# Kernel optimization log

Measured on AMD Instinct MI355X. Metric: run time of the kernel, lower is better.

Reference implementation:

```python
import jax, jax.numpy as jnp
import numpy as np

N = 60000      # total nodes (disjoint batch)
E = 240000     # total edges
F_IN = 10      # node feature dim
S = 3          # edge feature dim
C = 16         # nNodes (channel width)
G = 512        # number of graphs in batch


def setup_inputs() -> dict:
    key = jax.random.key(0)
    ks = jax.random.split(key, 24)
    sc = 0.05
    inp = {
        "x": jax.random.normal(ks[0], (N, F_IN), jnp.float32),
        "a_vals": jax.random.uniform(ks[1], (E,), jnp.float32),
        "e": jax.random.normal(ks[2], (E, S), jnp.float32),
        "edge_index": jax.random.randint(ks[3], (2, E), 0, N, jnp.int32),
        "seg": jnp.sort(jax.random.randint(ks[4], (N,), 0, G, jnp.int32)),
        # GCNConv 1/2
        "W_gcn1": jax.random.normal(ks[5], (F_IN, C), jnp.float32) * sc,
        "b_gcn1": jnp.zeros((C,), jnp.float32),
        "W_gcn2": jax.random.normal(ks[6], (C, 2 * C), jnp.float32) * sc,
        "b_gcn2": jnp.zeros((2 * C,), jnp.float32),
        # ECCConv 1 (edge kernel net: Dense(S -> F_IN*C), root kernel, bias)
        "We1": jax.random.normal(ks[7], (S, F_IN * C), jnp.float32) * sc,
        "be1": jnp.zeros((F_IN * C,), jnp.float32),
        "root1": jax.random.normal(ks[8], (F_IN, C), jnp.float32) * sc,
        "bias1": jnp.zeros((C,), jnp.float32),
        # ECCConv 2 (Dense(S -> C*2C))
        "We2": jax.random.normal(ks[9], (S, C * 2 * C), jnp.float32) * sc,
        "be2": jnp.zeros((C * 2 * C,), jnp.float32),
        "root2": jax.random.normal(ks[10], (C, 2 * C), jnp.float32) * sc,
        "bias2": jnp.zeros((2 * C,), jnp.float32),
        # MLP head: concat(2C + 2C) -> C -> C//2 -> 1
        "Wd1": jax.random.normal(ks[11], (4 * C, C), jnp.float32) * sc,
        "bd1": jnp.zeros((C,), jnp.float32),
        "Wd2": jax.random.normal(ks[12], (C, C // 2), jnp.float32) * sc,
        "bd2": jnp.zeros((C // 2,), jnp.float32),
        "Wo": jax.random.normal(ks[13], (C // 2, 1), jnp.float32) * sc,
        "bo": jnp.zeros((1,), jnp.float32),
    }
    return inp


def _spmm(rows, cols, vals, y):
    # sparse A @ y : out[i] += vals * y[j]
    return jax.ops.segment_sum(vals[:, None] * y[cols], rows, num_segments=N)


def _gcn(x, rows, cols, vals, W, b):
    return jax.nn.relu(_spmm(rows, cols, vals, x @ W) + b)


def _ecc(x, rows, cols, e, We, be, root, bias, f_in, f_out):
    # per-edge kernel matrix from edge features
    kern = (e @ We + be).reshape(-1, f_in, f_out)        # [E, Fin, Fout]
    msgs = jnp.einsum('ef,efo->eo', x[cols], kern)       # [E, Fout]
    agg = jax.ops.segment_sum(msgs, rows, num_segments=N)
    return jax.nn.relu(agg + x @ root + bias)


def reference(x, a_vals, e, edge_index, seg,
              W_gcn1, b_gcn1, W_gcn2, b_gcn2,
              We1, be1, root1, bias1,
              We2, be2, root2, bias2,
              Wd1, bd1, Wd2, bd2, Wo, bo):
    rows, cols = edge_index[0], edge_index[1]
    # GCN branch
    g1 = _gcn(x, rows, cols, a_vals, W_gcn1, b_gcn1)      # [N, C]
    g2 = _gcn(g1, rows, cols, a_vals, W_gcn2, b_gcn2)     # [N, 2C]
    # ECC branch
    c1 = _ecc(x, rows, cols, e, We1, be1, root1, bias1, F_IN, C)       # [N, C]
    c2 = _ecc(c1, rows, cols, e, We2, be2, root2, bias2, C, 2 * C)     # [N, 2C]
    # global sum pool per graph
    p1 = jax.ops.segment_sum(g2, seg, num_segments=G)     # [G, 2C]
    p2 = jax.ops.segment_sum(c2, seg, num_segments=G)     # [G, 2C]
    h = jnp.concatenate([p1, p2], axis=-1)                # [G, 4C]
    h = jax.nn.relu(h @ Wd1 + bd1)
    h = jax.nn.relu(h @ Wd2 + bd2)
    # dropout rate 0.0 -> identity (inference)
    return jax.nn.sigmoid(h @ Wo + bo)                    # [G, 1]
```

## Files before the change

### kernel.cpp

```cpp
#include <hip/hip_runtime.h>
#include <math.h>

#define N_NODES 60000
#define N_EDGES 240000
#define F_INQ 10
#define G_DIM 512
#define CAP 32
#define NB_EDGE ((N_EDGES + 255) / 256)
#define NB_TILE ((N_NODES + 63) / 64)
#define NB_E1  ((N_NODES * F_INQ + 255) / 256)
#define PQ1_STRIDE 56

__global__ __launch_bounds__(256) void k_build(
    const int* __restrict__ ei, const float* __restrict__ a_vals,
    const float* __restrict__ efeat,
    int* __restrict__ rs, int* __restrict__ ecol, float4* __restrict__ edata,
    const float* __restrict__ Wg1, const float* __restrict__ bg1,
    const float* __restrict__ We1, const float* __restrict__ be1,
    const float* __restrict__ root1, const float* __restrict__ bias1,
    const float* __restrict__ Wg2, const float* __restrict__ bg2,
    const float* __restrict__ We2, const float* __restrict__ be2,
    const float* __restrict__ root2, const float* __restrict__ bias2,
    float* __restrict__ Wt1, float* __restrict__ Wt2)
{
    if (blockIdx.x == NB_EDGE) {
        for (int i = threadIdx.x; i < 16 * 11; i += 256) {
            int o = i / 11, f = i - o * 11;
            Wt1[o * 64 + f] = (f < 10) ? Wg1[f * 16 + o] : bg1[o];
        }
        for (int i = threadIdx.x; i < 16 * 51; i += 256) {
            int o = i / 51, f = i - o * 51;
            float w;
            if      (f < 10) w = be1[f * 16 + o];
            else if (f < 20) w = We1[(f - 10) * 16 + o];
            else if (f < 30) w = We1[160 + (f - 20) * 16 + o];
            else if (f < 40) w = We1[320 + (f - 30) * 16 + o];
            else if (f < 50) w = root1[(f - 40) * 16 + o];
            else             w = bias1[o];
            Wt1[(16 + o) * 64 + f] = w;
        }
        return;
    }
    if (blockIdx.x == NB_EDGE + 1) {
        for (int i = threadIdx.x; i < 32 * 17; i += 256) {
            int o = i / 17, f = i - o * 17;
            Wt2[o * 96 + f] = (f < 16) ? Wg2[f * 32 + o] : bg2[o];
        }
        for (int i = threadIdx.x; i < 32 * 81; i += 256) {
            int o = i / 81, f = i - o * 81;
            float w;
            if      (f < 16) w = be2[f * 32 + o];
            else if (f < 32) w = We2[(f - 16) * 32 + o];
            else if (f < 48) w = We2[512 + (f - 32) * 32 + o];
            else if (f < 64) w = We2[1024 + (f - 48) * 32 + o];
            else if (f < 80) w = root2[(f - 64) * 32 + o];
            else             w = bias2[o];
            Wt2[(32 + o) * 96 + f] = w;
        }
        return;
    }

    int e = blockIdx.x * 256 + threadIdx.x;
    if (e >= N_EDGES) return;
    int row = ei[e];
    int slot = atomicAdd(&rs[row], 1);
    int idx = row * CAP + slot;
    ecol[idx] = ei[N_EDGES + e];
    edata[idx] = make_float4(a_vals[e], efeat[e * 3], efeat[e * 3 + 1], efeat[e * 3 + 2]);
}

__global__ __launch_bounds__(256) void k_edge1(
    const float* __restrict__ x,
    const int* __restrict__ rs,
    const int* __restrict__ ecol, const float4* __restrict__ edata,
    float* __restrict__ PQ1)
{
    int idx = blockIdx.x * 256 + threadIdx.x;
    if (idx >= N_NODES * F_INQ) return;
    int node = idx / F_INQ;
    int f = idx - node * F_INQ;
    int start = node * CAP;
    int end = start + rs[node];
    float p0 = 0.f, p1 = 0.f, p2 = 0.f, p3 = 0.f, q = 0.f;
    int k = start;
    for (; k + 2 <= end; k += 2) {
        int c0 = ecol[k], c1 = ecol[k + 1];
        float4 e0 = edata[k], e1 = edata[k + 1];
        float x0 = x[c0 * F_INQ + f];
        float x1 = x[c1 * F_INQ + f];
        p0 += x0;        p0 += x1;
        p1 += e0.y * x0; p1 += e1.y * x1;
        p2 += e0.z * x0; p2 += e1.z * x1;
        p3 += e0.w * x0; p3 += e1.w * x1;
        q  += e0.x * x0; q  += e1.x * x1;
    }
    if (k < end) {
        int c0 = ecol[k];
        float4 e0 = edata[k];
        float x0 = x[c0 * F_INQ + f];
        p0 += x0;
        p1 += e0.y * x0;
        p2 += e0.z * x0;
        p3 += e0.w * x0;
        q  += e0.x * x0;
    }
    float* P = PQ1 + (size_t)node * PQ1_STRIDE;
    P[f]      = p0;
    P[10 + f] = p1;
    P[20 + f] = p2;
    P[30 + f] = p3;
    P[40 + f] = q;
}

__global__ __launch_bounds__(256) void k_tf1(
    const float* __restrict__ PQ1,
    const float* __restrict__ x,
    const float* __restrict__ Wt1,
    float* __restrict__ gc)
{
    __shared__ float val[64][33];
    int tile = blockIdx.x;
    int lane = threadIdx.x & 63;
    int wv = __builtin_amdgcn_readfirstlane(threadIdx.x >> 6);
    int node = tile * 64 + lane;
    int nclamp = node < N_NODES ? node : N_NODES - 1;

    float pr[52];
    const float4* P4 = (const float4*)(PQ1 + (size_t)nclamp * PQ1_STRIDE);
#pragma unroll
    for (int i = 0; i < 13; ++i) {
        float4 t = P4[i];
        pr[i * 4] = t.x; pr[i * 4 + 1] = t.y; pr[i * 4 + 2] = t.z; pr[i * 4 + 3] = t.w;
    }
    float xs[10];
    const float2* X2 = (const float2*)(x + (size_t)nclamp * F_INQ);
#pragma unroll
    for (int i = 0; i < 5; ++i) {
        float2 t = X2[i];
        xs[i * 2] = t.x; xs[i * 2 + 1] = t.y;
    }

#pragma unroll
    for (int j = 0; j < 4; ++j) {
        const float* wr = Wt1 + (wv * 4 + j) * 64;
        float a = wr[10];
#pragma unroll
        for (int f = 0; f < 10; ++f) a = fmaf(wr[f], pr[40 + f], a);
        val[lane][(wv * 4 + j) * 2] = a > 0.f ? a : 0.f;
    }
#pragma unroll
    for (int j = 0; j < 4; ++j) {
        const float* wr = Wt1 + (16 + wv * 4 + j) * 64;
        float a = wr[50];
#pragma unroll
        for (int f = 0; f < 40; ++f) a = fmaf(wr[f], pr[f], a);
#pragma unroll
        for (int f = 0; f < 10; ++f) a = fmaf(wr[40 + f], xs[f], a);
        val[lane][(wv * 4 + j) * 2 + 1] = a > 0.f ? a : 0.f;
    }
    __syncthreads();

    float4* G4 = (float4*)(gc + (size_t)tile * 64 * 32);
#pragma unroll
    for (int k = 0; k < 2; ++k) {
        int fi4 = k * 256 + threadIdx.x;
        int n = fi4 >> 3, o4 = (fi4 & 7) * 4;
        if (tile * 64 + n < N_NODES)
            G4[fi4] = make_float4(val[n][o4], val[n][o4 + 1], val[n][o4 + 2], val[n][o4 + 3]);
    }
}

__global__ __launch_bounds__(256) void k_edge2(
    const float* __restrict__ gc,
    const int* __restrict__ rs,
    const int* __restrict__ ecol, const float4* __restrict__ edata,
    float* __restrict__ PQ2)
{
    int idx = blockIdx.x * 256 + threadIdx.x;
    int node = idx >> 4, f = idx & 15;
    int start = node * CAP;
    int end = start + rs[node];
    const float2* GC2 = (const float2*)gc;
    float p0 = 0.f, p1 = 0.f, p2 = 0.f, p3 = 0.f, q = 0.f;
    int k = start;
    for (; k + 2 <= end; k += 2) {
        int c0 = ecol[k], c1 = ecol[k + 1];
        float4 e0 = edata[k], e1 = edata[k + 1];
        float2 t0 = GC2[c0 * 16 + f];
        float2 t1 = GC2[c1 * 16 + f];
        p0 += t0.y;        p0 += t1.y;
        p1 += e0.y * t0.y; p1 += e1.y * t1.y;
        p2 += e0.z * t0.y; p2 += e1.z * t1.y;
        p3 += e0.w * t0.y; p3 += e1.w * t1.y;
        q  += e0.x * t0.x; q  += e1.x * t1.x;
    }
    if (k < end) {
        int c0 = ecol[k];
        float4 e0 = edata[k];
        float2 t0 = GC2[c0 * 16 + f];
        p0 += t0.y;
        p1 += e0.y * t0.y;
        p2 += e0.z * t0.y;
        p3 += e0.w * t0.y;
        q  += e0.x * t0.x;
    }
    float* P = PQ2 + (size_t)node * 80;
    P[f]      = p0;
    P[16 + f] = p1;
    P[32 + f] = p2;
    P[48 + f] = p3;
    P[64 + f] = q;
}

__global__ __launch_bounds__(256) void k_tf2pool(
    const float* __restrict__ PQ2,
    const float* __restrict__ gc,
    const int* __restrict__ seg,
    const float* __restrict__ Wt2,
    float* __restrict__ pool)
{
    __shared__ float val[64][65];
    __shared__ int sseg[64];
    int tile = blockIdx.x;
    int lane = threadIdx.x & 63;
    int wv = __builtin_amdgcn_readfirstlane(threadIdx.x >> 6);
    int node = tile * 64 + lane;
    int nclamp = node < N_NODES ? node : N_NODES - 1;

    if (threadIdx.x < 64) {
        int nd = tile * 64 + threadIdx.x;
        sseg[threadIdx.x] = (nd < N_NODES) ? seg[nd] : -1;
    }

    float pr[80];
    const float4* P4 = (const float4*)(PQ2 + (size_t)nclamp * 80);
#pragma unroll
    for (int i = 0; i < 20; ++i) {
        float4 t = P4[i];
        pr[i * 4] = t.x; pr[i * 4 + 1] = t.y; pr[i * 4 + 2] = t.z; pr[i * 4 + 3] = t.w;
    }
    float cs[16];
    const float4* C4 = (const float4*)(gc + (size_t)nclamp * 32);
#pragma unroll
    for (int i = 0; i < 8; ++i) {
        float4 t = C4[i];
        cs[i * 2] = t.y; cs[i * 2 + 1] = t.w;
    }

#pragma unroll
    for (int j = 0; j < 8; ++j) {
        const float* wr = Wt2 + (wv * 8 + j) * 96;
        float a = wr[16];
#pragma unroll
        for (int f = 0; f < 16; ++f) a = fmaf(wr[f], pr[64 + f], a);
        val[lane][wv * 8 + j] = a > 0.f ? a : 0.f;
    }
#pragma unroll
    for (int j = 0; j < 8; ++j) {
        const float* wr = Wt2 + (32 + wv * 8 + j) * 96;
        float a = wr[80];
#pragma unroll
        for (int f = 0; f < 64; ++f) a = fmaf(wr[f], pr[f], a);
#pragma unroll
        for (int f = 0; f < 16; ++f) a = fmaf(wr[64 + f], cs[f], a);
        val[lane][32 + wv * 8 + j] = a > 0.f ? a : 0.f;
    }
    __syncthreads();

    int c = threadIdx.x & 63, q = threadIdx.x >> 6;
    int base = q * 16;
    float acc = 0.f;
    int curg = -1;
    for (int n = 0; n < 16; ++n) {
        int nd = tile * 64 + base + n;
        if (nd >= N_NODES) break;
        int gsg = sseg[base + n];
        if (gsg != curg) {
            if (curg >= 0) atomicAdd(&pool[curg * 64 + c], acc);
            acc = 0.f;
            curg = gsg;
        }
        acc += val[base + n][c];
    }
    if (curg >= 0) atomicAdd(&pool[curg * 64 + c], acc);
}

__global__ __launch_bounds__(256) void k_head(
    const float* __restrict__ pool,
    const float* __restrict__ Wd1, const float* __restrict__ bd1,
    const float* __restrict__ Wd2, const float* __restrict__ bd2,
    const float* __restrict__ Wo,  const float* __restrict__ bo,
    float* __restrict__ out)
{
    __shared__ float pl[4][64];
    __shared__ float h1s[4][16];
    __shared__ float h2s[4][8];
    int q = threadIdx.x >> 6, t = threadIdx.x & 63;
    int g = blockIdx.x * 4 + q;
    pl[q][t] = pool[g * 64 + t];
    __syncthreads();
    if (t < 16) {
        float a = bd1[t];
        for (int k = 0; k < 64; ++k) a += pl[q][k] * Wd1[k * 16 + t];
        h1s[q][t] = a > 0.f ? a : 0.f;
    }
    __syncthreads();
    if (t < 8) {
        float a = bd2[t];
        for (int k = 0; k < 16; ++k) a += h1s[q][k] * Wd2[k * 8 + t];
        h2s[q][t] = a > 0.f ? a : 0.f;
    }
    __syncthreads();
    if (t == 0) {
        float a = bo[0];
        for (int k = 0; k < 8; ++k) a += h2s[q][k] * Wo[k];
        out[g] = 1.f / (1.f + expf(-a));
    }
}

extern "C" void kernel_launch(void* const* d_in, const int* in_sizes, int n_in,
                              void* d_out, int out_size, void* d_ws, size_t ws_size,
                              hipStream_t stream)
{
    const float* x      = (const float*)d_in[0];
    const float* a_vals = (const float*)d_in[1];
    const float* efeat  = (const float*)d_in[2];
    const int*   ei     = (const int*)d_in[3];
    const int*   seg    = (const int*)d_in[4];
    const float* Wg1    = (const float*)d_in[5];
    const float* bg1    = (const float*)d_in[6];
    const float* Wg2    = (const float*)d_in[7];
    const float* bg2    = (const float*)d_in[8];
    const float* We1    = (const float*)d_in[9];
    const float* be1    = (const float*)d_in[10];
    const float* root1  = (const float*)d_in[11];
    const float* bias1  = (const float*)d_in[12];
    const float* We2    = (const float*)d_in[13];
    const float* be2    = (const float*)d_in[14];
    const float* root2  = (const float*)d_in[15];
    const float* bias2  = (const float*)d_in[16];
    const float* Wd1    = (const float*)d_in[17];
    const float* bd1    = (const float*)d_in[18];
    const float* Wd2    = (const float*)d_in[19];
    const float* bd2    = (const float*)d_in[20];
    const float* Wo     = (const float*)d_in[21];
    const float* bo     = (const float*)d_in[22];

    float4* edata = (float4*)d_ws;
    float*  PQ1  = (float*)(edata + (size_t)N_NODES * CAP);
    float*  gc   = PQ1 + (size_t)N_NODES * PQ1_STRIDE;
    float*  PQ2  = gc + (size_t)N_NODES * 32;
    float*  Wt1  = PQ2 + (size_t)N_NODES * 80;
    float*  Wt2  = Wt1 + 32 * 64;
    int*    rs   = (int*)(Wt2 + 64 * 96);
    float*  pool = (float*)(rs + N_NODES);
    int*    ecol = (int*)(pool + (size_t)G_DIM * 64);
    float*  out  = (float*)d_out;

    hipMemsetAsync(rs, 0, sizeof(int) * (N_NODES + G_DIM * 64), stream);

    k_build<<<NB_EDGE + 2, 256, 0, stream>>>(ei, a_vals, efeat, rs, ecol, edata,
                                             Wg1, bg1, We1, be1, root1, bias1,
                                             Wg2, bg2, We2, be2, root2, bias2,
                                             Wt1, Wt2);

    k_edge1<<<NB_E1, 256, 0, stream>>>(x, rs, ecol, edata, PQ1);
    k_tf1  <<<NB_TILE, 256, 0, stream>>>(PQ1, x, Wt1, gc);

    k_edge2<<<N_NODES * 16 / 256, 256, 0, stream>>>(gc, rs, ecol, edata, PQ2);
    k_tf2pool<<<NB_TILE, 256, 0, stream>>>(PQ2, gc, seg, Wt2, pool);

    k_head<<<G_DIM / 4, 256, 0, stream>>>(pool, Wd1, bd1, Wd2, bd2, Wo, bo, out);
}
```

Baseline: 178.5 us.

## Fuse layer-1 edge aggregation and node transform into one kernel

Merges k_edge1 and k_tf1 into a single k_l1 kernel. Each node is handled by a 16-lane group: lanes gather the per-feature aggregates, then exchange them through shuffles to compute the 16 GCN and 16 ECC outputs directly. Layer-1 weights are staged in shared memory per block, so the Wt1 preprocessing and the PQ1 intermediate buffer are removed, saving a launch and a global round trip. In exchange, 6 of every 16 lanes sit idle during the gather phase, and every block reloads the weights into shared memory.

Result: no change. 181.1 us (+1.5%).

```diff
diff --git a/kernel.cpp b/kernel.cpp
--- a/kernel.cpp
+++ b/kernel.cpp
@@ -8,40 +8,18 @@
 #define CAP 32
 #define NB_EDGE ((N_EDGES + 255) / 256)
 #define NB_TILE ((N_NODES + 63) / 64)
-#define NB_E1  ((N_NODES * F_INQ + 255) / 256)
-#define PQ1_STRIDE 56
+#define NB_L1  (N_NODES / 16)
 
 __global__ __launch_bounds__(256) void k_build(
     const int* __restrict__ ei, const float* __restrict__ a_vals,
     const float* __restrict__ efeat,
     int* __restrict__ rs, int* __restrict__ ecol, float4* __restrict__ edata,
-    const float* __restrict__ Wg1, const float* __restrict__ bg1,
-    const float* __restrict__ We1, const float* __restrict__ be1,
-    const float* __restrict__ root1, const float* __restrict__ bias1,
     const float* __restrict__ Wg2, const float* __restrict__ bg2,
     const float* __restrict__ We2, const float* __restrict__ be2,
     const float* __restrict__ root2, const float* __restrict__ bias2,
-    float* __restrict__ Wt1, float* __restrict__ Wt2)
+    float* __restrict__ Wt2)
 {
     if (blockIdx.x == NB_EDGE) {
-        for (int i = threadIdx.x; i < 16 * 11; i += 256) {
-            int o = i / 11, f = i - o * 11;
-            Wt1[o * 64 + f] = (f < 10) ? Wg1[f * 16 + o] : bg1[o];
-        }
-        for (int i = threadIdx.x; i < 16 * 51; i += 256) {
-            int o = i / 51, f = i - o * 51;
-            float w;
-            if      (f < 10) w = be1[f * 16 + o];
-            else if (f < 20) w = We1[(f - 10) * 16 + o];
-            else if (f < 30) w = We1[160 + (f - 20) * 16 + o];
-            else if (f < 40) w = We1[320 + (f - 30) * 16 + o];
-            else if (f < 50) w = root1[(f - 40) * 16 + o];
-            else             w = bias1[o];
-            Wt1[(16 + o) * 64 + f] = w;
-        }
-        return;
-    }
-    if (blockIdx.x == NB_EDGE + 1) {
         for (int i = threadIdx.x; i < 32 * 17; i += 256) {
             int o = i / 17, f = i - o * 17;
             Wt2[o * 96 + f] = (f < 16) ? Wg2[f * 32 + o] : bg2[o];
@@ -69,105 +47,79 @@
     edata[idx] = make_float4(a_vals[e], efeat[e * 3], efeat[e * 3 + 1], efeat[e * 3 + 2]);
 }
 
-__global__ __launch_bounds__(256) void k_edge1(
+__global__ __launch_bounds__(256) void k_l1(
     const float* __restrict__ x,
     const int* __restrict__ rs,
     const int* __restrict__ ecol, const float4* __restrict__ edata,
-    float* __restrict__ PQ1)
-{
-    int idx = blockIdx.x * 256 + threadIdx.x;
-    if (idx >= N_NODES * F_INQ) return;
-    int node = idx / F_INQ;
-    int f = idx - node * F_INQ;
-    int start = node * CAP;
-    int end = start + rs[node];
-    float p0 = 0.f, p1 = 0.f, p2 = 0.f, p3 = 0.f, q = 0.f;
-    int k = start;
-    for (; k + 2 <= end; k += 2) {
-        int c0 = ecol[k], c1 = ecol[k + 1];
-        float4 e0 = edata[k], e1 = edata[k + 1];
-        float x0 = x[c0 * F_INQ + f];
-        float x1 = x[c1 * F_INQ + f];
-        p0 += x0;        p0 += x1;
-        p1 += e0.y * x0; p1 += e1.y * x1;
-        p2 += e0.z * x0; p2 += e1.z * x1;
-        p3 += e0.w * x0; p3 += e1.w * x1;
-        q  += e0.x * x0; q  += e1.x * x1;
-    }
-    if (k < end) {
-        int c0 = ecol[k];
-        float4 e0 = edata[k];
-        float x0 = x[c0 * F_INQ + f];
-        p0 += x0;
-        p1 += e0.y * x0;
-        p2 += e0.z * x0;
-        p3 += e0.w * x0;
-        q  += e0.x * x0;
-    }
-    float* P = PQ1 + (size_t)node * PQ1_STRIDE;
-    P[f]      = p0;
-    P[10 + f] = p1;
-    P[20 + f] = p2;
-    P[30 + f] = p3;
-    P[40 + f] = q;
-}
-
-__global__ __launch_bounds__(256) void k_tf1(
-    const float* __restrict__ PQ1,
-    const float* __restrict__ x,
-    const float* __restrict__ Wt1,
+    const float* __restrict__ Wg1, const float* __restrict__ bg1,
+    const float* __restrict__ We1, const float* __restrict__ be1,
+    const float* __restrict__ root1, const float* __restrict__ bias1,
     float* __restrict__ gc)
 {
-    __shared__ float val[64][33];
-    int tile = blockIdx.x;
-    int lane = threadIdx.x & 63;
-    int wv = __builtin_amdgcn_readfirstlane(threadIdx.x >> 6);
-    int node = tile * 64 + lane;
-    int nclamp = node < N_NODES ? node : N_NODES - 1;
-
-    float pr[52];
-    const float4* P4 = (const float4*)(PQ1 + (size_t)nclamp * PQ1_STRIDE);
-#pragma unroll
-    for (int i = 0; i < 13; ++i) {
-        float4 t = P4[i];
-        pr[i * 4] = t.x; pr[i * 4 + 1] = t.y; pr[i * 4 + 2] = t.z; pr[i * 4 + 3] = t.w;
-    }
-    float xs[10];
-    const float2* X2 = (const float2*)(x + (size_t)nclamp * F_INQ);
-#pragma unroll
-    for (int i = 0; i < 5; ++i) {
-        float2 t = X2[i];
-        xs[i * 2] = t.x; xs[i * 2 + 1] = t.y;
-    }
-
-#pragma unroll
-    for (int j = 0; j < 4; ++j) {
-        const float* wr = Wt1 + (wv * 4 + j) * 64;
-        float a = wr[10];
-#pragma unroll
-        for (int f = 0; f < 10; ++f) a = fmaf(wr[f], pr[40 + f], a);
-        val[lane][(wv * 4 + j) * 2] = a > 0.f ? a : 0.f;
-    }
-#pragma unroll
-    for (int j = 0; j < 4; ++j) {
-        const float* wr = Wt1 + (16 + wv * 4 + j) * 64;
-        float a = wr[50];
-#pragma unroll
-        for (int f = 0; f < 40; ++f) a = fmaf(wr[f], pr[f], a);
-#pragma unroll
-        for (int f = 0; f < 10; ++f) a = fmaf(wr[40 + f], xs[f], a);
-        val[lane][(wv * 4 + j) * 2 + 1] = a > 0.f ? a : 0.f;
-    }
-    __syncthreads();
-
-    float4* G4 = (float4*)(gc + (size_t)tile * 64 * 32);
-#pragma unroll
-    for (int k = 0; k < 2; ++k) {
-        int fi4 = k * 256 + threadIdx.x;
-        int n = fi4 >> 3, o4 = (fi4 & 7) * 4;
-        if (tile * 64 + n < N_NODES)
-            G4[fi4] = make_float4(val[n][o4], val[n][o4 + 1], val[n][o4 + 2], val[n][o4 + 3]);
-    }
+    __shared__ float w[992];
+    for (int t = threadIdx.x; t < 992; t += 256) {
+        float v;
+        if (t < 960) {
+            int slot = t / 160, r = t - slot * 160;
+            if (slot == 0)      v = Wg1[r];
+            else if (slot <= 3) v = We1[(slot - 1) * 160 + r];
+            else if (slot == 4) v = be1[r];
+            else                v = root1[r];
+        } else if (t < 976) v = bias1[t - 960];
+        else                v = bg1[t - 976];
+        w[t] = v;
+    }
+    __syncthreads();
+
+    int o = threadIdx.x & 15;
+    int grp = threadIdx.x >> 4;
+    int node = blockIdx.x * 16 + grp;
+
+    float p0 = 0.f, p1 = 0.f, p2 = 0.f, p3 = 0.f, q = 0.f, xv = 0.f;
+    if (o < F_INQ) {
+        int start = node * CAP;
+        int end = start + rs[node];
+        int k = start;
+        for (; k + 2 <= end; k += 2) {
+            int c0 = ecol[k], c1 = ecol[k + 1];
+            float4 e0 = edata[k], e1 = edata[k + 1];
+            float x0 = x[c0 * F_INQ + o];
+            float x1 = x[c1 * F_INQ + o];
+            p0 += x0;        p0 += x1;
+            p1 += e0.y * x0; p1 += e1.y * x1;
+            p2 += e0.z * x0; p2 += e1.z * x1;
+            p3 += e0.w * x0; p3 += e1.w * x1;
+            q  += e0.x * x0; q  += e1.x * x1;
+        }
+        if (k < end) {
+            int c0 = ecol[k];
+            float4 e0 = edata[k];
+            float x0 = x[c0 * F_INQ + o];
+            p0 += x0;
+            p1 += e0.y * x0;
+            p2 += e0.z * x0;
+            p3 += e0.w * x0;
+            q  += e0.x * x0;
+        }
+        xv = x[node * F_INQ + o];
+    }
+
+    float ac = w[960 + o], ag = w[976 + o];
+#pragma unroll
+    for (int f = 0; f < 10; ++f) {
+        float P0 = __shfl(p0, f, 16);
+        float P1 = __shfl(p1, f, 16);
+        float P2 = __shfl(p2, f, 16);
+        float P3 = __shfl(p3, f, 16);
+        float Qf = __shfl(q,  f, 16);
+        float Xf = __shfl(xv, f, 16);
+        ac += P0 * w[640 + f * 16 + o] + P1 * w[160 + f * 16 + o]
+            + P2 * w[320 + f * 16 + o] + P3 * w[480 + f * 16 + o]
+            + Xf * w[800 + f * 16 + o];
+        ag += Qf * w[f * 16 + o];
+    }
+    float2 r2 = make_float2(ag > 0.f ? ag : 0.f, ac > 0.f ? ac : 0.f);
+    *(float2*)(gc + (size_t)node * 32 + 2 * o) = r2;
 }
 
 __global__ __launch_bounds__(256) void k_edge2(
@@ -347,11 +299,9 @@
     const float* bo     = (const float*)d_in[22];
 
     float4* edata = (float4*)d_ws;
-    float*  PQ1  = (float*)(edata + (size_t)N_NODES * CAP);
-    float*  gc   = PQ1 + (size_t)N_NODES * PQ1_STRIDE;
+    float*  gc   = (float*)(edata + (size_t)N_NODES * CAP);
     float*  PQ2  = gc + (size_t)N_NODES * 32;
-    float*  Wt1  = PQ2 + (size_t)N_NODES * 80;
-    float*  Wt2  = Wt1 + 32 * 64;
+    float*  Wt2  = PQ2 + (size_t)N_NODES * 80;
     int*    rs   = (int*)(Wt2 + 64 * 96);
     float*  pool = (float*)(rs + N_NODES);
     int*    ecol = (int*)(pool + (size_t)G_DIM * 64);
@@ -359,13 +309,11 @@
 
     hipMemsetAsync(rs, 0, sizeof(int) * (N_NODES + G_DIM * 64), stream);
 
-    k_build<<<NB_EDGE + 2, 256, 0, stream>>>(ei, a_vals, efeat, rs, ecol, edata,
-                                             Wg1, bg1, We1, be1, root1, bias1,
-                                             Wg2, bg2, We2, be2, root2, bias2,
-                                             Wt1, Wt2);
-
-    k_edge1<<<NB_E1, 256, 0, stream>>>(x, rs, ecol, edata, PQ1);
-    k_tf1  <<<NB_TILE, 256, 0, stream>>>(PQ1, x, Wt1, gc);
+    k_build<<<NB_EDGE + 1, 256, 0, stream>>>(ei, a_vals, efeat, rs, ecol, edata,
+                                             Wg2, bg2, We2, be2, root2, bias2, Wt2);
+
+    k_l1<<<NB_L1, 256, 0, stream>>>(x, rs, ecol, edata,
+                                    Wg1, bg1, We1, be1, root1, bias1, gc);
 
     k_edge2<<<N_NODES * 16 / 256, 256, 0, stream>>>(gc, rs, ecol, edata, PQ2);
     k_tf2pool<<<NB_TILE, 256, 0, stream>>>(PQ2, gc, seg, Wt2, pool);
```
